# Optimization experiments

Hardware: AMD Instinct MI355X
Metric: run time of the kernel (lower is better)

Reference implementation:

```python
import jax, jax.numpy as jnp
import numpy as np

N_LANGS = 2
VOCAB = 200000
DIM = 300
B = 1024
S = 50
EPS = 1e-5  # BatchNorm1d default eps


def _bn(x):
    # BatchNorm1d(affine=False) in training mode: per-batch stats, biased variance
    return (x - x.mean(axis=0)) / jnp.sqrt(x.var(axis=0) + EPS)


def setup_inputs() -> dict:
    key = jax.random.key(0)
    ks = jax.random.split(key, 16)
    # frozen per-language embedding tables, stacked: [n_langs, vocab, dim]
    tables = jax.random.normal(ks[0], (N_LANGS, VOCAB, DIM), jnp.float32) * 0.1
    tables = tables.at[:, 0, :].set(0.0)  # padding_idx=0 row
    langs_1 = jax.random.randint(ks[1], (B,), 0, N_LANGS, dtype=jnp.int32)
    langs_2 = jax.random.randint(ks[2], (B,), 0, N_LANGS, dtype=jnp.int32)
    sents_1 = jax.random.randint(ks[3], (B, S), 0, VOCAB, dtype=jnp.int64)
    sents_2 = jax.random.randint(ks[4], (B, S), 0, VOCAB, dtype=jnp.int64)
    # lin1/lin2 initialized to identity in the original module
    w1 = jnp.eye(DIM, dtype=jnp.float32)
    b1 = jax.random.uniform(ks[5], (DIM,), jnp.float32, -0.05, 0.05)
    w2 = jnp.eye(DIM, dtype=jnp.float32)
    b2 = jax.random.uniform(ks[6], (DIM,), jnp.float32, -0.05, 0.05)
    w3 = jax.random.normal(ks[7], (400, 901), jnp.float32) * 0.03
    b3 = jax.random.uniform(ks[8], (400,), jnp.float32, -0.03, 0.03)
    w4 = jax.random.normal(ks[9], (100, 400), jnp.float32) * 0.05
    b4 = jax.random.uniform(ks[10], (100,), jnp.float32, -0.05, 0.05)
    w5 = jax.random.normal(ks[11], (1, 100), jnp.float32) * 0.1
    b5 = jax.random.uniform(ks[12], (1,), jnp.float32, -0.1, 0.1)
    return {
        "langs_1": langs_1, "sents_1": sents_1,
        "langs_2": langs_2, "sents_2": sents_2,
        "tables": tables,
        "w1": w1, "b1": b1, "w2": w2, "b2": b2,
        "w3": w3, "b3": b3, "w4": w4, "b4": b4,
        "w5": w5, "b5": b5,
    }


def reference(langs_1, sents_1, langs_2, sents_2, tables,
              w1, b1, w2, b2, w3, b3, w4, b4, w5, b5):
    # batched table-select + embedding lookup + sum-pool (replaces the per-sample loop)
    x1 = tables[langs_1[:, None], sents_1].sum(axis=1)  # [B, 300]
    x2 = tables[langs_2[:, None], sents_2].sum(axis=1)  # [B, 300]

    def enc(x):
        h = jax.nn.relu(_bn(x @ w1.T + b1))
        return jax.nn.relu(_bn(h @ w2.T + b2))

    o1 = enc(x1)
    o2 = enc(x2)
    cor = jnp.sum(o1 * o2, axis=1, keepdims=True)          # [B, 1]
    nxt = jnp.concatenate([o1, o2, jnp.abs(o1 - o2), cor], axis=1)  # [B, 901]
    h = jax.nn.relu(_bn(nxt @ w3.T + b3))                  # [B, 400]
    h = jax.nn.relu(_bn(h @ w4.T + b4))                    # [B, 100]
    score = h @ w5.T + b5                                  # [B, 1]
    prob = jax.nn.sigmoid(score)
    return prob, o1, o2
```

## Files before the change

### kernel.cpp

```cpp
#include <hip/hip_runtime.h>
#include <math.h>

#define EPS 1e-5f
#define INV_N (1.0f / 1024.0f)


typedef _Float16 f16x8 __attribute__((ext_vector_type(8)));
typedef float f32x4 __attribute__((ext_vector_type(4)));

__device__ __forceinline__ _Float16 f2h(float f) { return (_Float16)f; }

static const int STATS_TOTAL = 3400;

__global__ __launch_bounds__(128) void gather_kernel(
    const int* __restrict__ langs1, const int* __restrict__ sents1,
    const int* __restrict__ langs2, const int* __restrict__ sents2,
    const float* __restrict__ tables, _Float16* __restrict__ xb,
    float* __restrict__ stats)
{
    int idx = blockIdx.x, t = threadIdx.x;
    if (idx == 0) {
        for (int i = t; i < STATS_TOTAL; i += 128) stats[i] = 0.f;
    }
    int side = idx >> 10, b = idx & 1023;
    const int* langs = side ? langs2 : langs1;
    const int* sents = side ? sents2 : sents1;
    __shared__ int toks[50];
    if (t < 50) toks[t] = sents[b * 50 + t];
    __syncthreads();
    const float* base = tables + (size_t)langs[b] * (200000ull * 300ull);
    float a0 = 0.f, a1 = 0.f, a2 = 0.f;
    #pragma unroll 5
    for (int s = 0; s < 50; s++) {
        const float* row = base + (size_t)toks[s] * 300;
        a0 += row[t];
        a1 += row[t + 128];
        if (t < 44) a2 += row[t + 256];
    }
    _Float16* xr = xb + (size_t)idx * 320;
    xr[t] = f2h(a0);
    xr[t + 128] = f2h(a1);
    if (t < 64) xr[t + 256] = (t < 44) ? f2h(a2) : (_Float16)0.f;
}

__global__ __launch_bounds__(256) void wcvt_kernel(
    const float* __restrict__ w1, const float* __restrict__ w2,
    const float* __restrict__ w3, const float* __restrict__ w4,
    _Float16* __restrict__ w1b, _Float16* __restrict__ w2b,
    _Float16* __restrict__ w3b, _Float16* __restrict__ w4b)
{
    int i = blockIdx.x * 256 + threadIdx.x;
    if (i < 102400) {
        int r = i / 320, c = i - r * 320;
        w1b[i] = (r < 300 && c < 300) ? f2h(w1[r * 300 + c]) : (_Float16)0.f;
    } else if (i < 204800) {
        int j = i - 102400; int r = j / 320, c = j - r * 320;
        w2b[j] = (r < 300 && c < 300) ? f2h(w2[r * 300 + c]) : (_Float16)0.f;
    } else if (i < 620544) {
        int j = i - 204800; int r = j / 928, c = j - r * 928;
        w3b[j] = (r < 400 && c < 901) ? f2h(w3[r * 901 + c]) : (_Float16)0.f;
    } else if (i < 673792) {
        int j = i - 620544; int r = j / 416, c = j - r * 416;
        w4b[j] = (r < 100 && c < 400) ? f2h(w4[r * 400 + c]) : (_Float16)0.f;
    }
}

__global__ __launch_bounds__(256) void gemm_f16(
    const _Float16* __restrict__ A, const _Float16* __restrict__ W, int ldk,
    const float* __restrict__ bias, float* __restrict__ C, int ldc,
    int N, int kIters, float* __restrict__ sSum, float* __restrict__ sSq,
    int twoSided)
{
    __shared__ __align__(16) _Float16 lsA[2048];
    __shared__ __align__(16) _Float16 lsW[2048];
    int tid = threadIdx.x;
    int r0 = blockIdx.x * 64, c0 = blockIdx.y * 64;
    int lane = tid & 63;
    int wave = tid >> 6;
    int waveR = wave & 1, waveC = wave >> 1;
    int q = lane >> 4, m = lane & 15;

    int srow = tid >> 2, sseg = tid & 3;
    const _Float16* gA = A + (size_t)(r0 + srow) * ldk + sseg * 8;
    const _Float16* gW = W + (size_t)(c0 + srow) * ldk + sseg * 8;
    _Float16* stA = &lsA[sseg * 512 + srow * 8];
    _Float16* stW = &lsW[sseg * 512 + srow * 8];

    int aoff0 = q * 512 + (waveR * 32 + m) * 8;
    int aoff1 = aoff0 + 128;
    int boff0 = q * 512 + (waveC * 32 + m) * 8;
    int boff1 = boff0 + 128;

    f32x4 acc00 = {0.f,0.f,0.f,0.f}, acc01 = {0.f,0.f,0.f,0.f};
    f32x4 acc10 = {0.f,0.f,0.f,0.f}, acc11 = {0.f,0.f,0.f,0.f};

    for (int kt = 0; kt < kIters; kt++) {
        uint4 va = *(const uint4*)gA;
        uint4 vw = *(const uint4*)gW;
        gA += 32; gW += 32;
        __syncthreads();
        *(uint4*)stA = va;
        *(uint4*)stW = vw;
        __syncthreads();
        f16x8 a0 = *(const f16x8*)&lsA[aoff0];
        f16x8 a1 = *(const f16x8*)&lsA[aoff1];
        f16x8 b0 = *(const f16x8*)&lsW[boff0];
        f16x8 b1 = *(const f16x8*)&lsW[boff1];
        acc00 = __builtin_amdgcn_mfma_f32_16x16x32_f16(a0, b0, acc00, 0, 0, 0);
        acc01 = __builtin_amdgcn_mfma_f32_16x16x32_f16(a0, b1, acc01, 0, 0, 0);
        acc10 = __builtin_amdgcn_mfma_f32_16x16x32_f16(a1, b0, acc10, 0, 0, 0);
        acc11 = __builtin_amdgcn_mfma_f32_16x16x32_f16(a1, b1, acc11, 0, 0, 0);
    }

    int side = (twoSided && r0 >= 1024) ? 1 : 0;
    int gc0 = c0 + waveC * 32 + m;
    int gc1 = gc0 + 16;
    float bias0 = (gc0 < N) ? bias[gc0] : 0.f;
    float bias1 = (gc1 < N) ? bias[gc1] : 0.f;
    float colS0 = 0.f, colQ0 = 0.f, colS1 = 0.f, colQ1 = 0.f;
    #pragma unroll
    for (int i = 0; i < 2; i++) {
        f32x4 cv0 = i ? acc10 : acc00;
        f32x4 cv1 = i ? acc11 : acc01;
        #pragma unroll
        for (int r = 0; r < 4; r++) {
            int gr = r0 + waveR * 32 + i * 16 + q * 4 + r;
            if (gc0 < N) {
                float v = cv0[r] + bias0;
                C[(size_t)gr * ldc + gc0] = v;
                colS0 += v; colQ0 += v * v;
            }
            if (gc1 < N) {
                float v = cv1[r] + bias1;
                C[(size_t)gr * ldc + gc1] = v;
                colS1 += v; colQ1 += v * v;
            }
        }
    }
    colS0 += __shfl_down(colS0, 32); colS0 += __shfl_down(colS0, 16);
    colQ0 += __shfl_down(colQ0, 32); colQ0 += __shfl_down(colQ0, 16);
    colS1 += __shfl_down(colS1, 32); colS1 += __shfl_down(colS1, 16);
    colQ1 += __shfl_down(colQ1, 32); colQ1 += __shfl_down(colQ1, 16);
    if (q == 0) {
        if (gc0 < N) {
            atomicAdd(&sSum[side * N + gc0], colS0);
            atomicAdd(&sSq[side * N + gc0], colQ0);
        }
        if (gc1 < N) {
            atomicAdd(&sSum[side * N + gc1], colS1);
            atomicAdd(&sSq[side * N + gc1], colQ1);
        }
    }
}

__global__ __launch_bounds__(256) void bncvt1_kernel(
    const float* __restrict__ z, const float* __restrict__ sS,
    const float* __restrict__ sQ, _Float16* __restrict__ out)
{
    int i = blockIdx.x * 256 + threadIdx.x;
    int r = i / 320, c = i - r * 320;
    _Float16 v = (_Float16)0.f;
    if (c < 300) {
        int side = r >> 10;
        float mean = sS[side * 300 + c] * INV_N;
        float var  = sQ[side * 300 + c] * INV_N - mean * mean;
        float x = (z[r * 300 + c] - mean) * rsqrtf(var + EPS);
        v = f2h(fmaxf(x, 0.f));
    }
    out[i] = v;
}

__global__ __launch_bounds__(256) void bncvt3_kernel(
    const float* __restrict__ z, const float* __restrict__ sS,
    const float* __restrict__ sQ, _Float16* __restrict__ out)
{
    int i = blockIdx.x * 256 + threadIdx.x;
    int r = i / 416, c = i - r * 416;
    _Float16 v = (_Float16)0.f;
    if (c < 400) {
        float mean = sS[c] * INV_N;
        float var  = sQ[c] * INV_N - mean * mean;
        float x = (z[r * 400 + c] - mean) * rsqrtf(var + EPS);
        v = f2h(fmaxf(x, 0.f));
    }
    out[i] = v;
}

__global__ __launch_bounds__(128) void pair_kernel(
    const float* __restrict__ z2, const float* __restrict__ sS,
    const float* __restrict__ sQ, float* __restrict__ out,
    _Float16* __restrict__ nxtb)
{
    int b = blockIdx.x, t = threadIdx.x;
    __shared__ float red[128];
    float dot = 0.f;
    for (int d = t; d < 300; d += 128) {
        float m1 = sS[d] * INV_N;
        float v1 = sQ[d] * INV_N - m1 * m1;
        float m2 = sS[300 + d] * INV_N;
        float v2 = sQ[300 + d] * INV_N - m2 * m2;
        float a1 = fmaxf((z2[(size_t)b * 300 + d] - m1) * rsqrtf(v1 + EPS), 0.f);
        float a2 = fmaxf((z2[(size_t)(1024 + b) * 300 + d] - m2) * rsqrtf(v2 + EPS), 0.f);
        out[1024 + (size_t)b * 300 + d] = a1;
        out[308224 + (size_t)b * 300 + d] = a2;
        nxtb[(size_t)b * 928 + d] = f2h(a1);
        nxtb[(size_t)b * 928 + 300 + d] = f2h(a2);
        nxtb[(size_t)b * 928 + 600 + d] = f2h(fabsf(a1 - a2));
        dot += a1 * a2;
    }
    red[t] = dot;
    __syncthreads();
    if (t < 27) nxtb[(size_t)b * 928 + 901 + t] = (_Float16)0.f;
    if (t == 0) {
        float s = 0.f;
        for (int i = 0; i < 128; i++) s += red[i];
        nxtb[(size_t)b * 928 + 900] = f2h(s);
    }
}

__global__ __launch_bounds__(64) void final_kernel(
    const float* __restrict__ y4, const float* __restrict__ sS,
    const float* __restrict__ sQ, const float* __restrict__ w5,
    const float* __restrict__ b5, float* __restrict__ out)
{
    int b = blockIdx.x, l = threadIdx.x;
    float acc = 0.f;
    for (int j = l; j < 100; j += 64) {
        float mean = sS[j] * INV_N;
        float var = sQ[j] * INV_N - mean * mean;
        float v = (y4[(size_t)b * 100 + j] - mean) * rsqrtf(var + EPS);
        v = v > 0.f ? v : 0.f;
        acc += v * w5[j];
    }
    #pragma unroll
    for (int off = 32; off; off >>= 1) acc += __shfl_down(acc, off);
    if (l == 0) out[b] = 1.f / (1.f + expf(-(acc + b5[0])));
}

extern "C" void kernel_launch(void* const* d_in, const int* in_sizes, int n_in,
                              void* d_out, int out_size, void* d_ws, size_t ws_size,
                              hipStream_t stream)
{
    const int* langs1 = (const int*)d_in[0];
    const int* sents1 = (const int*)d_in[1];
    const int* langs2 = (const int*)d_in[2];
    const int* sents2 = (const int*)d_in[3];
    const float* tables = (const float*)d_in[4];
    const float* w1 = (const float*)d_in[5];
    const float* b1 = (const float*)d_in[6];
    const float* w2 = (const float*)d_in[7];
    const float* b2 = (const float*)d_in[8];
    const float* w3 = (const float*)d_in[9];
    const float* b3 = (const float*)d_in[10];
    const float* w4 = (const float*)d_in[11];
    const float* b4 = (const float*)d_in[12];
    const float* w5 = (const float*)d_in[13];
    const float* b5 = (const float*)d_in[14];

    float* ws = (float*)d_ws;
    float* F0 = ws;
    float* F1 = ws + 614400;
    float* stats = ws + 1228800;
    float* s1S = stats;        float* s1Q = stats + 600;
    float* s2S = stats + 1200; float* s2Q = stats + 1800;
    float* s3S = stats + 2400; float* s3Q = stats + 2800;
    float* s4S = stats + 3200; float* s4Q = stats + 3300;
    _Float16* hb = (_Float16*)(ws + 1232208);
    _Float16* xb   = hb;
    _Float16* a1b  = hb + 655360;
    _Float16* nxtb = hb + 1310720;
    _Float16* a3b  = hb + 2260992;
    _Float16* w1b  = hb + 2686976;
    _Float16* w2b  = hb + 2789376;
    _Float16* w3b  = hb + 2891776;
    _Float16* w4b  = hb + 3307520;

    float* out = (float*)d_out;

    gather_kernel<<<2048, 128, 0, stream>>>(langs1, sents1, langs2, sents2,
                                            tables, xb, stats);
    wcvt_kernel<<<2632, 256, 0, stream>>>(w1, w2, w3, w4, w1b, w2b, w3b, w4b);
    gemm_f16<<<dim3(32, 5), 256, 0, stream>>>(xb, w1b, 320, b1, F0, 300,
                                              300, 10, s1S, s1Q, 1);
    bncvt1_kernel<<<2560, 256, 0, stream>>>(F0, s1S, s1Q, a1b);
    gemm_f16<<<dim3(32, 5), 256, 0, stream>>>(a1b, w2b, 320, b2, F1, 300,
                                              300, 10, s2S, s2Q, 1);
    pair_kernel<<<1024, 128, 0, stream>>>(F1, s2S, s2Q, out, nxtb);
    gemm_f16<<<dim3(16, 7), 256, 0, stream>>>(nxtb, w3b, 928, b3, F0, 400,
                                              400, 29, s3S, s3Q, 0);
    bncvt3_kernel<<<1664, 256, 0, stream>>>(F0, s3S, s3Q, a3b);
    gemm_f16<<<dim3(16, 2), 256, 0, stream>>>(a3b, w4b, 416, b4, F1, 100,
                                              100, 13, s4S, s4Q, 0);
    final_kernel<<<1024, 64, 0, stream>>>(F1, s4S, s4Q, w5, b5, out);
}
```

Measured before the change: 643.6 us.

## Fuse BN-ReLU into GEMM A-loads, double-buffer LDS, merge gather with weight convert

```diff
diff --git a/kernel.cpp b/kernel.cpp
--- a/kernel.cpp
+++ b/kernel.cpp
@@ -12,17 +12,42 @@
 
 static const int STATS_TOTAL = 3400;
 
-__global__ __launch_bounds__(128) void gather_kernel(
+__global__ __launch_bounds__(128) void gather_wcvt_kernel(
     const int* __restrict__ langs1, const int* __restrict__ sents1,
     const int* __restrict__ langs2, const int* __restrict__ sents2,
     const float* __restrict__ tables, _Float16* __restrict__ xb,
-    float* __restrict__ stats)
-{
-    int idx = blockIdx.x, t = threadIdx.x;
-    if (idx == 0) {
+    float* __restrict__ stats,
+    const float* __restrict__ w1, const float* __restrict__ w2,
+    const float* __restrict__ w3, const float* __restrict__ w4,
+    _Float16* __restrict__ w1b, _Float16* __restrict__ w2b,
+    _Float16* __restrict__ w3b, _Float16* __restrict__ w4b)
+{
+    int bid = blockIdx.x, t = threadIdx.x;
+    if (bid >= 2048) {
+        int i0 = (bid - 2048) * 512 + t;
+        #pragma unroll
+        for (int u = 0; u < 4; u++) {
+            int i = i0 + u * 128;
+            if (i < 102400) {
+                int r = i / 320, c = i - r * 320;
+                w1b[i] = (r < 300 && c < 300) ? f2h(w1[r * 300 + c]) : (_Float16)0.f;
+            } else if (i < 204800) {
+                int j = i - 102400; int r = j / 320, c = j - r * 320;
+                w2b[j] = (r < 300 && c < 300) ? f2h(w2[r * 300 + c]) : (_Float16)0.f;
+            } else if (i < 620544) {
+                int j = i - 204800; int r = j / 928, c = j - r * 928;
+                w3b[j] = (r < 400 && c < 901) ? f2h(w3[r * 901 + c]) : (_Float16)0.f;
+            } else if (i < 673792) {
+                int j = i - 620544; int r = j / 416, c = j - r * 416;
+                w4b[j] = (r < 100 && c < 400) ? f2h(w4[r * 400 + c]) : (_Float16)0.f;
+            }
+        }
+        return;
+    }
+    if (bid == 0) {
         for (int i = t; i < STATS_TOTAL; i += 128) stats[i] = 0.f;
     }
-    int side = idx >> 10, b = idx & 1023;
+    int side = bid >> 10, b = bid & 1023;
     const int* langs = side ? langs2 : langs1;
     const int* sents = side ? sents2 : sents1;
     __shared__ int toks[50];
@@ -37,32 +62,10 @@
         a1 += row[t + 128];
         if (t < 44) a2 += row[t + 256];
     }
-    _Float16* xr = xb + (size_t)idx * 320;
+    _Float16* xr = xb + (size_t)bid * 320;
     xr[t] = f2h(a0);
     xr[t + 128] = f2h(a1);
     if (t < 64) xr[t + 256] = (t < 44) ? f2h(a2) : (_Float16)0.f;
-}
-
-__global__ __launch_bounds__(256) void wcvt_kernel(
-    const float* __restrict__ w1, const float* __restrict__ w2,
-    const float* __restrict__ w3, const float* __restrict__ w4,
-    _Float16* __restrict__ w1b, _Float16* __restrict__ w2b,
-    _Float16* __restrict__ w3b, _Float16* __restrict__ w4b)
-{
-    int i = blockIdx.x * 256 + threadIdx.x;
-    if (i < 102400) {
-        int r = i / 320, c = i - r * 320;
-        w1b[i] = (r < 300 && c < 300) ? f2h(w1[r * 300 + c]) : (_Float16)0.f;
-    } else if (i < 204800) {
-        int j = i - 102400; int r = j / 320, c = j - r * 320;
-        w2b[j] = (r < 300 && c < 300) ? f2h(w2[r * 300 + c]) : (_Float16)0.f;
-    } else if (i < 620544) {
-        int j = i - 204800; int r = j / 928, c = j - r * 928;
-        w3b[j] = (r < 400 && c < 901) ? f2h(w3[r * 901 + c]) : (_Float16)0.f;
-    } else if (i < 673792) {
-        int j = i - 620544; int r = j / 416, c = j - r * 416;
-        w4b[j] = (r < 100 && c < 400) ? f2h(w4[r * 400 + c]) : (_Float16)0.f;
-    }
 }
 
 __global__ __launch_bounds__(256) void gemm_f16(
@@ -71,8 +74,8 @@
     int N, int kIters, float* __restrict__ sSum, float* __restrict__ sSq,
     int twoSided)
 {
-    __shared__ __align__(16) _Float16 lsA[2048];
-    __shared__ __align__(16) _Float16 lsW[2048];
+    __shared__ __align__(16) _Float16 lsA[2][2048];
+    __shared__ __align__(16) _Float16 lsW[2][2048];
     int tid = threadIdx.x;
     int r0 = blockIdx.x * 64, c0 = blockIdx.y * 64;
     int lane = tid & 63;
@@ -83,8 +86,7 @@
     int srow = tid >> 2, sseg = tid & 3;
     const _Float16* gA = A + (size_t)(r0 + srow) * ldk + sseg * 8;
     const _Float16* gW = W + (size_t)(c0 + srow) * ldk + sseg * 8;
-    _Float16* stA = &lsA[sseg * 512 + srow * 8];
-    _Float16* stW = &lsW[sseg * 512 + srow * 8];
+    int stOff = sseg * 512 + srow * 8;
 
     int aoff0 = q * 512 + (waveR * 32 + m) * 8;
     int aoff1 = aoff0 + 128;
@@ -94,22 +96,37 @@
     f32x4 acc00 = {0.f,0.f,0.f,0.f}, acc01 = {0.f,0.f,0.f,0.f};
     f32x4 acc10 = {0.f,0.f,0.f,0.f}, acc11 = {0.f,0.f,0.f,0.f};
 
+    uint4 va = *(const uint4*)gA;
+    uint4 vw = *(const uint4*)gW;
+    gA += 32; gW += 32;
+    *(uint4*)&lsA[0][stOff] = va;
+    *(uint4*)&lsW[0][stOff] = vw;
+    if (kIters > 1) {
+        va = *(const uint4*)gA; vw = *(const uint4*)gW;
+        gA += 32; gW += 32;
+    }
+    __syncthreads();
+
+    int cur = 0;
     for (int kt = 0; kt < kIters; kt++) {
-        uint4 va = *(const uint4*)gA;
-        uint4 vw = *(const uint4*)gW;
-        gA += 32; gW += 32;
-        __syncthreads();
-        *(uint4*)stA = va;
-        *(uint4*)stW = vw;
-        __syncthreads();
-        f16x8 a0 = *(const f16x8*)&lsA[aoff0];
-        f16x8 a1 = *(const f16x8*)&lsA[aoff1];
-        f16x8 b0 = *(const f16x8*)&lsW[boff0];
-        f16x8 b1 = *(const f16x8*)&lsW[boff1];
+        f16x8 a0 = *(const f16x8*)&lsA[cur][aoff0];
+        f16x8 a1 = *(const f16x8*)&lsA[cur][aoff1];
+        f16x8 b0 = *(const f16x8*)&lsW[cur][boff0];
+        f16x8 b1 = *(const f16x8*)&lsW[cur][boff1];
         acc00 = __builtin_amdgcn_mfma_f32_16x16x32_f16(a0, b0, acc00, 0, 0, 0);
         acc01 = __builtin_amdgcn_mfma_f32_16x16x32_f16(a0, b1, acc01, 0, 0, 0);
         acc10 = __builtin_amdgcn_mfma_f32_16x16x32_f16(a1, b0, acc10, 0, 0, 0);
         acc11 = __builtin_amdgcn_mfma_f32_16x16x32_f16(a1, b1, acc11, 0, 0, 0);
+        if (kt + 1 < kIters) {
+            *(uint4*)&lsA[cur ^ 1][stOff] = va;
+            *(uint4*)&lsW[cur ^ 1][stOff] = vw;
+            if (kt + 2 < kIters) {
+                va = *(const uint4*)gA; vw = *(const uint4*)gW;
+                gA += 32; gW += 32;
+            }
+            __syncthreads();
+        }
+        cur ^= 1;
     }
 
     int side = (twoSided && r0 >= 1024) ? 1 : 0;
@@ -153,37 +170,142 @@
     }
 }
 
-__global__ __launch_bounds__(256) void bncvt1_kernel(
-    const float* __restrict__ z, const float* __restrict__ sS,
-    const float* __restrict__ sQ, _Float16* __restrict__ out)
-{
-    int i = blockIdx.x * 256 + threadIdx.x;
-    int r = i / 320, c = i - r * 320;
-    _Float16 v = (_Float16)0.f;
-    if (c < 300) {
-        int side = r >> 10;
-        float mean = sS[side * 300 + c] * INV_N;
-        float var  = sQ[side * 300 + c] * INV_N - mean * mean;
-        float x = (z[r * 300 + c] - mean) * rsqrtf(var + EPS);
-        v = f2h(fmaxf(x, 0.f));
-    }
-    out[i] = v;
-}
-
-__global__ __launch_bounds__(256) void bncvt3_kernel(
-    const float* __restrict__ z, const float* __restrict__ sS,
-    const float* __restrict__ sQ, _Float16* __restrict__ out)
-{
-    int i = blockIdx.x * 256 + threadIdx.x;
-    int r = i / 416, c = i - r * 416;
-    _Float16 v = (_Float16)0.f;
-    if (c < 400) {
-        float mean = sS[c] * INV_N;
-        float var  = sQ[c] * INV_N - mean * mean;
-        float x = (z[r * 400 + c] - mean) * rsqrtf(var + EPS);
-        v = f2h(fmaxf(x, 0.f));
-    }
-    out[i] = v;
+__global__ __launch_bounds__(256) void gemm_bnA(
+    const float* __restrict__ Z, int ldz, int kValid,
+    const float* __restrict__ bnS, const float* __restrict__ bnQ, int bnTwoSided,
+    const _Float16* __restrict__ W, int ldk,
+    const float* __restrict__ bias, float* __restrict__ C, int ldc,
+    int N, int kIters, float* __restrict__ sSum, float* __restrict__ sSq,
+    int twoSided)
+{
+    __shared__ __align__(16) _Float16 lsA[2][2048];
+    __shared__ __align__(16) _Float16 lsW[2][2048];
+    int tid = threadIdx.x;
+    int r0 = blockIdx.x * 64, c0 = blockIdx.y * 64;
+    int lane = tid & 63;
+    int wave = tid >> 6;
+    int waveR = wave & 1, waveC = wave >> 1;
+    int q = lane >> 4, m = lane & 15;
+
+    int srow = tid >> 2, sseg = tid & 3;
+    int bnSide = (bnTwoSided && r0 >= 1024) ? 1 : 0;
+    const float* bS = bnS + bnSide * kValid;
+    const float* bQ = bnQ + bnSide * kValid;
+    const float* gZ = Z + (size_t)(r0 + srow) * ldz + sseg * 8;
+    const _Float16* gW = W + (size_t)(c0 + srow) * ldk + sseg * 8;
+    int stOff = sseg * 512 + srow * 8;
+
+    int aoff0 = q * 512 + (waveR * 32 + m) * 8;
+    int aoff1 = aoff0 + 128;
+    int boff0 = q * 512 + (waveC * 32 + m) * 8;
+    int boff1 = boff0 + 128;
+
+    f32x4 acc00 = {0.f,0.f,0.f,0.f}, acc01 = {0.f,0.f,0.f,0.f};
+    f32x4 acc10 = {0.f,0.f,0.f,0.f}, acc11 = {0.f,0.f,0.f,0.f};
+
+    float4 z0, z1, s0, s1, u0, u1;
+    uint4 vw;
+    int kcol = sseg * 8;
+
+    #define LOAD_BNA(kt_) do {                                             \
+        int cb = (kt_) * 32 + kcol;                                        \
+        z0 = *(const float4*)(gZ + (kt_) * 32);                            \
+        z1 = *(const float4*)(gZ + (kt_) * 32 + 4);                        \
+        s0 = *(const float4*)(bS + cb);                                    \
+        s1 = *(const float4*)(bS + cb + 4);                                \
+        u0 = *(const float4*)(bQ + cb);                                    \
+        u1 = *(const float4*)(bQ + cb + 4);                                \
+        vw = *(const uint4*)(gW + (size_t)(kt_) * 32);                     \
+    } while (0)
+
+    #define STORE_BNA(buf_, kt_) do {                                      \
+        int cb = (kt_) * 32 + kcol;                                        \
+        f16x8 h;                                                           \
+        _Pragma("unroll")                                                  \
+        for (int j = 0; j < 8; j++) {                                      \
+            int c = cb + j;                                                \
+            float v = 0.f;                                                 \
+            if (c < kValid) {                                              \
+                float sv = (j < 4) ? ((const float*)&s0)[j]                \
+                                   : ((const float*)&s1)[j - 4];           \
+                float qv = (j < 4) ? ((const float*)&u0)[j]                \
+                                   : ((const float*)&u1)[j - 4];           \
+                float zv = (j < 4) ? ((const float*)&z0)[j]                \
+                                   : ((const float*)&z1)[j - 4];           \
+                float mean = sv * INV_N;                                   \
+                float var  = qv * INV_N - mean * mean;                     \
+                v = fmaxf((zv - mean) * rsqrtf(var + EPS), 0.f);           \
+            }                                                              \
+            h[j] = f2h(v);                                                 \
+        }                                                                  \
+        *(f16x8*)&lsA[buf_][stOff] = h;                                    \
+        *(uint4*)&lsW[buf_][stOff] = vw;                                   \
+    } while (0)
+
+    LOAD_BNA(0);
+    STORE_BNA(0, 0);
+    if (kIters > 1) LOAD_BNA(1);
+    __syncthreads();
+
+    int cur = 0;
+    for (int kt = 0; kt < kIters; kt++) {
+        f16x8 a0 = *(const f16x8*)&lsA[cur][aoff0];
+        f16x8 a1 = *(const f16x8*)&lsA[cur][aoff1];
+        f16x8 b0 = *(const f16x8*)&lsW[cur][boff0];
+        f16x8 b1 = *(const f16x8*)&lsW[cur][boff1];
+        acc00 = __builtin_amdgcn_mfma_f32_16x16x32_f16(a0, b0, acc00, 0, 0, 0);
+        acc01 = __builtin_amdgcn_mfma_f32_16x16x32_f16(a0, b1, acc01, 0, 0, 0);
+        acc10 = __builtin_amdgcn_mfma_f32_16x16x32_f16(a1, b0, acc10, 0, 0, 0);
+        acc11 = __builtin_amdgcn_mfma_f32_16x16x32_f16(a1, b1, acc11, 0, 0, 0);
+        if (kt + 1 < kIters) {
+            STORE_BNA(cur ^ 1, kt + 1);
+            if (kt + 2 < kIters) LOAD_BNA(kt + 2);
+            __syncthreads();
+        }
+        cur ^= 1;
+    }
+    #undef LOAD_BNA
+    #undef STORE_BNA
+
+    int side = (twoSided && r0 >= 1024) ? 1 : 0;
+    int gc0 = c0 + waveC * 32 + m;
+    int gc1 = gc0 + 16;
+    float bias0 = (gc0 < N) ? bias[gc0] : 0.f;
+    float bias1 = (gc1 < N) ? bias[gc1] : 0.f;
+    float colS0 = 0.f, colQ0 = 0.f, colS1 = 0.f, colQ1 = 0.f;
+    #pragma unroll
+    for (int i = 0; i < 2; i++) {
+        f32x4 cv0 = i ? acc10 : acc00;
+        f32x4 cv1 = i ? acc11 : acc01;
+        #pragma unroll
+        for (int r = 0; r < 4; r++) {
+            int gr = r0 + waveR * 32 + i * 16 + q * 4 + r;
+            if (gc0 < N) {
+                float v = cv0[r] + bias0;
+                C[(size_t)gr * ldc + gc0] = v;
+                colS0 += v; colQ0 += v * v;
+            }
+            if (gc1 < N) {
+                float v = cv1[r] + bias1;
+                C[(size_t)gr * ldc + gc1] = v;
+                colS1 += v; colQ1 += v * v;
+            }
+        }
+    }
+    colS0 += __shfl_down(colS0, 32); colS0 += __shfl_down(colS0, 16);
+    colQ0 += __shfl_down(colQ0, 32); colQ0 += __shfl_down(colQ0, 16);
+    colS1 += __shfl_down(colS1, 32); colS1 += __shfl_down(colS1, 16);
+    colQ1 += __shfl_down(colQ1, 32); colQ1 += __shfl_down(colQ1, 16);
+    if (q == 0) {
+        if (gc0 < N) {
+            atomicAdd(&sSum[side * N + gc0], colS0);
+            atomicAdd(&sSq[side * N + gc0], colQ0);
+        }
+        if (gc1 < N) {
+            atomicAdd(&sSum[side * N + gc1], colS1);
+            atomicAdd(&sSq[side * N + gc1], colQ1);
+        }
+    }
 }
 
 __global__ __launch_bounds__(128) void pair_kernel(
@@ -267,9 +389,7 @@
     float* s4S = stats + 3200; float* s4Q = stats + 3300;
     _Float16* hb = (_Float16*)(ws + 1232208);
     _Float16* xb   = hb;
-    _Float16* a1b  = hb + 655360;
     _Float16* nxtb = hb + 1310720;
-    _Float16* a3b  = hb + 2260992;
     _Float16* w1b  = hb + 2686976;
     _Float16* w2b  = hb + 2789376;
     _Float16* w3b  = hb + 2891776;
@@ -277,19 +397,19 @@
 
     float* out = (float*)d_out;
 
-    gather_kernel<<<2048, 128, 0, stream>>>(langs1, sents1, langs2, sents2,
-                                            tables, xb, stats);
-    wcvt_kernel<<<2632, 256, 0, stream>>>(w1, w2, w3, w4, w1b, w2b, w3b, w4b);
+    gather_wcvt_kernel<<<3364, 128, 0, stream>>>(
+        langs1, sents1, langs2, sents2, tables, xb, stats,
+        w1, w2, w3, w4, w1b, w2b, w3b, w4b);
     gemm_f16<<<dim3(32, 5), 256, 0, stream>>>(xb, w1b, 320, b1, F0, 300,
                                               300, 10, s1S, s1Q, 1);
-    bncvt1_kernel<<<2560, 256, 0, stream>>>(F0, s1S, s1Q, a1b);
-    gemm_f16<<<dim3(32, 5), 256, 0, stream>>>(a1b, w2b, 320, b2, F1, 300,
+    gemm_bnA<<<dim3(32, 5), 256, 0, stream>>>(F0, 300, 300, s1S, s1Q, 1,
+                                              w2b, 320, b2, F1, 300,
                                               300, 10, s2S, s2Q, 1);
     pair_kernel<<<1024, 128, 0, stream>>>(F1, s2S, s2Q, out, nxtb);
     gemm_f16<<<dim3(16, 7), 256, 0, stream>>>(nxtb, w3b, 928, b3, F0, 400,
                                               400, 29, s3S, s3Q, 0);
-    bncvt3_kernel<<<1664, 256, 0, stream>>>(F0, s3S, s3Q, a3b);
-    gemm_f16<<<dim3(16, 2), 256, 0, stream>>>(a3b, w4b, 416, b4, F1, 100,
+    gemm_bnA<<<dim3(16, 2), 256, 0, stream>>>(F0, 400, 400, s3S, s3Q, 0,
+                                              w4b, 416, b4, F1, 100,
                                               100, 13, s4S, s4Q, 0);
     final_kernel<<<1024, 64, 0, stream>>>(F1, s4S, s4Q, w5, b5, out);
 }
```

Result: no change. 639.9 us (-0.6%).
